# Kernel optimization log

Measured on AMD Instinct MI355X. Metric: run time of the kernel, lower is better.

## Reference

```python
import jax, jax.numpy as jnp
import numpy as np
import math

L = 6          # num_layers
D = 512        # hidden_dim
S = 2048       # seq_len
B = 8          # batch
ODIM = 1       # output_dim
SCALES = (24.0, 720.0)


def setup_inputs() -> dict:
    key = jax.random.key(0)
    ks = jax.random.split(key, 12)
    def n(k, shape, scale=0.02):
        return jax.random.normal(k, shape, dtype=jnp.float32) * scale
    return {
        "z": jax.random.normal(ks[0], (B, S, 1), dtype=jnp.float32),
        "c": jax.random.normal(ks[1], (B, S, 1), dtype=jnp.float32),
        "enc_w": n(ks[2], (D, 2)), "enc_b": jnp.zeros((D,), jnp.float32),
        "beta": jnp.ones((L, len(SCALES)), jnp.float32),
        "wq": n(ks[3], (L, D, D)), "bq": jnp.zeros((L, D), jnp.float32),
        "wk": n(ks[4], (L, D, D)), "bk": jnp.zeros((L, D), jnp.float32),
        "wv": n(ks[5], (L, D, D)), "bv": jnp.zeros((L, D), jnp.float32),
        "ln1_w": jnp.ones((L, D), jnp.float32), "ln1_b": jnp.zeros((L, D), jnp.float32),
        "ln2_w": jnp.ones((L, D), jnp.float32), "ln2_b": jnp.zeros((L, D), jnp.float32),
        "ff1_w": n(ks[6], (L, 4 * D, D)), "ff1_b": jnp.zeros((L, 4 * D), jnp.float32),
        "ff2_w": n(ks[7], (L, D, 4 * D)), "ff2_b": jnp.zeros((L, D), jnp.float32),
        "out_w": n(ks[8], (ODIM, D)), "out_b": jnp.zeros((ODIM,), jnp.float32),
    }


def _ln(x, w, b, eps=1e-5):
    m = jnp.mean(x, axis=-1, keepdims=True)
    v = jnp.var(x, axis=-1, keepdims=True)
    return (x - m) * jax.lax.rsqrt(v + eps) * w + b


def _posenc(seq_len, dim):
    pos = jnp.arange(seq_len, dtype=jnp.float32)[:, None]
    div = jnp.exp(jnp.arange(0, dim, 2, dtype=jnp.float32) * (-(math.log(10000.0) / dim)))
    pe = jnp.zeros((seq_len, dim), jnp.float32)
    pe = pe.at[:, 0::2].set(jnp.sin(pos * div))
    pe = pe.at[:, 1::2].set(jnp.cos(pos * div))
    return pe


def reference(z, c, enc_w, enc_b, beta, wq, bq, wk, bk, wv, bv,
              ln1_w, ln1_b, ln2_w, ln2_b, ff1_w, ff1_b, ff2_w, ff2_b,
              out_w, out_b):
    # SequenceEncoder: cat(z,c) -> Linear(2, D) -> + sinusoidal PE
    x = jnp.concatenate([z, c], axis=-1) @ enc_w.T + enc_b       # [B,S,D]
    seq_len, d = x.shape[1], x.shape[2]
    x = x + _posenc(seq_len, d)[None]
    sqrt_d = math.sqrt(d)

    idx = jnp.arange(seq_len, dtype=jnp.float32)
    dist = jnp.abs(idx[:, None] - idx[None, :])                  # [S,S]

    for l in range(L):
        # pre-norm with ln1 (applied twice in the original code - replicated)
        xn = _ln(x, ln1_w[l], ln1_b[l])
        Q = xn @ wq[l].T + bq[l]
        K = xn @ wk[l].T + bk[l]
        V = xn @ wv[l].T + bv[l]
        attn = jnp.einsum('bid,bjd->bij', Q, K) / sqrt_d          # [B,S,S]
        bias = beta[l, 0] * jnp.cos(2.0 * math.pi * dist / SCALES[0]) \
             + beta[l, 1] * jnp.cos(2.0 * math.pi * dist / SCALES[1])
        probs = jax.nn.softmax(attn + bias, axis=-1)
        att_out = jnp.einsum('bij,bjd->bid', probs, V)
        # original applies layer_norm_1 again to the residual sum
        x = _ln(x + att_out, ln1_w[l], ln1_b[l])
        xn2 = _ln(x, ln2_w[l], ln2_b[l])
        h = jax.nn.relu(xn2 @ ff1_w[l].T + ff1_b[l])
        x = x + h @ ff2_w[l].T + ff2_b[l]

    return x @ out_w.T + out_b                                    # [B,S,ODIM]
```

## Files before the change

### kernel.cpp

```cpp
#include <hip/hip_runtime.h>
#include <hip/hip_fp8.h>
#include <math.h>

#define BB 8
#define SS 2048
#define DD 512
#define LL 6
#define FFD 2048

typedef _Float16 half_t;
typedef __attribute__((ext_vector_type(8))) _Float16 half8;
typedef __attribute__((ext_vector_type(4))) float f32x4;

enum { EPI_NONE = 0, EPI_RELU = 2, EPI_RES = 3, EPI_ATTN = 4, EPI_QKV = 5, EPI_PV = 6 };

__device__ __forceinline__ unsigned char f2e4m3(float v) {
    __hip_fp8_e4m3 f(v);
    return f.__x;
}

__device__ __forceinline__ void gl_lds16(const void* g, void* l) {
    __builtin_amdgcn_global_load_lds(
        (const __attribute__((address_space(1))) unsigned int*)g,
        (__attribute__((address_space(3))) unsigned int*)l,
        16, 0, 0);
}

__device__ __forceinline__ void blockReduce2(float& a, float& b, float* sm) {
#pragma unroll
    for (int off = 32; off; off >>= 1) {
        a += __shfl_down(a, off);
        b += __shfl_down(b, off);
    }
    int lane = threadIdx.x & 63;
    int w = threadIdx.x >> 6;
    if (lane == 0) { sm[w] = a; sm[4 + w] = b; }
    __syncthreads();
    a = sm[0] + sm[1] + sm[2] + sm[3];
    b = sm[4] + sm[5] + sm[6] + sm[7];
    __syncthreads();
}

__global__ __launch_bounds__(256) void encode_kernel(
    const float* __restrict__ z, const float* __restrict__ c,
    const float* __restrict__ enc_w, const float* __restrict__ enc_b,
    float* __restrict__ x)
{
    int idx = blockIdx.x * 256 + threadIdx.x;
    int d  = idx & (DD - 1);
    int bs = idx >> 9;
    int s  = bs & (SS - 1);
    float v = z[bs] * enc_w[2 * d] + c[bs] * enc_w[2 * d + 1] + enc_b[d];
    float div = expf(-(float)(d & ~1) * (9.210340371976184f / 512.0f));
    float ang = (float)s * div;
    v += (d & 1) ? cosf(ang) : sinf(ang);
    x[idx] = v;
}

__global__ __launch_bounds__(256) void convert_ff_all_kernel(
    const float* __restrict__ f1, const float* __restrict__ f2,
    half_t* __restrict__ f1h, half_t* __restrict__ f2h)
{
    const size_t NF = (size_t)LL * FFD * DD;
    size_t i = (size_t)blockIdx.x * 256 + threadIdx.x;
    if (i < NF) f1h[i] = (half_t)f1[i];
    else        f2h[i - NF] = (half_t)f2[i - NF];
}

__global__ __launch_bounds__(256) void convert_qkv_kernel(
    const float* __restrict__ wq, const float* __restrict__ wk,
    const float* __restrict__ wv, half_t* __restrict__ wqkv)
{
    const int NQ = DD * DD;
    int i = blockIdx.x * 256 + threadIdx.x;
    int which = i >> 18, j = i & (NQ - 1);
    const float* s = (which == 0) ? wq : (which == 1) ? wk : wv;
    wqkv[i] = (half_t)s[j];
}

__global__ __launch_bounds__(256) void bias_table_kernel(
    const float* __restrict__ beta, float* __restrict__ tbl)
{
    int i = blockIdx.x * 256 + threadIdx.x;
    int l = i >> 11, d = i & (SS - 1);
    tbl[i] = beta[2 * l] * cosf(0.2617993877991494f * d)
           + beta[2 * l + 1] * cosf(0.008726646259971648f * d);
}

__global__ __launch_bounds__(256) void ln_kernel(
    const float* __restrict__ src, const float* __restrict__ w,
    const float* __restrict__ b, half_t* __restrict__ dst)
{
    __shared__ float sm[8];
    size_t row = blockIdx.x;
    const float* p = src + row * DD;
    int t = threadIdx.x;
    float v0 = p[t], v1 = p[t + 256];
    float s = v0 + v1, sq = v0 * v0 + v1 * v1;
    blockReduce2(s, sq, sm);
    float mean = s * (1.0f / DD);
    float var  = sq * (1.0f / DD) - mean * mean;
    float rs   = rsqrtf(var + 1e-5f);
    dst[row * DD + t]       = (half_t)((v0 - mean) * rs * w[t] + b[t]);
    dst[row * DD + t + 256] = (half_t)((v1 - mean) * rs * w[t + 256] + b[t + 256]);
}

__global__ __launch_bounds__(256) void ln_ln_kernel(
    float* __restrict__ x,
    const float* __restrict__ w1, const float* __restrict__ b1,
    const float* __restrict__ w2, const float* __restrict__ b2,
    half_t* __restrict__ xn)
{
    __shared__ float sm[8];
    size_t row = blockIdx.x;
    int t = threadIdx.x;
    float v0 = x[row * DD + t];
    float v1 = x[row * DD + t + 256];
    float s = v0 + v1, sq = v0 * v0 + v1 * v1;
    blockReduce2(s, sq, sm);
    float mean = s * (1.0f / DD);
    float var  = sq * (1.0f / DD) - mean * mean;
    float rs   = rsqrtf(var + 1e-5f);
    float y0 = (v0 - mean) * rs * w1[t] + b1[t];
    float y1 = (v1 - mean) * rs * w1[t + 256] + b1[t + 256];
    x[row * DD + t]       = y0;
    x[row * DD + t + 256] = y1;
    s = y0 + y1; sq = y0 * y0 + y1 * y1;
    blockReduce2(s, sq, sm);
    mean = s * (1.0f / DD);
    var  = sq * (1.0f / DD) - mean * mean;
    rs   = rsqrtf(var + 1e-5f);
    xn[row * DD + t]       = (half_t)((y0 - mean) * rs * w2[t] + b2[t]);
    xn[row * DD + t + 256] = (half_t)((y1 - mean) * rs * w2[t + 256] + b2[t + 256]);
}

template<typename TIN, int MT, int EPI, int SWZ = 0>
__global__ __launch_bounds__(256) void gemm_mfma(
    const void* __restrict__ Ap, const void* __restrict__ Wp,
    const float* __restrict__ bias, void* __restrict__ Cp,
    int N, int K, int Kst, float alpha,
    long long sA, long long sW, long long sC,
    const float* __restrict__ biasK, const float* __restrict__ biasV,
    unsigned char* __restrict__ Ck, unsigned char* __restrict__ Cv)
{
    constexpr int TM = MT / 32;
    constexpr int ES = (int)sizeof(TIN);
    constexpr int NS = 64 / (32 * ES);
    constexpr int ABYTES = MT * 64;
    constexpr int BBYTES = 128 * 64;
    __shared__ __align__(16) unsigned char As[2 * ABYTES];
    __shared__ __align__(16) unsigned char Bs[2 * BBYTES];

    int bxi, byi, bzi;
    if (SWZ == 1) {
        const int id = blockIdx.x;
        const int cc = id & 7, rr = id >> 3;
        bxi = rr & 15;
        const int ss = cc + 8 * (rr >> 4);
        byi = ss & 15; bzi = ss >> 4;
    } else { bxi = blockIdx.x; byi = blockIdx.y; bzi = blockIdx.z; }

    const int z = bzi;
    const unsigned char* A = (const unsigned char*)Ap + (size_t)z * sA * ES;
    const unsigned char* W = (const unsigned char*)Wp + (size_t)z * sW * ES;
    float*  Cf = (float*)Cp  + (size_t)z * sC;
    half_t* Ch = (half_t*)Cp + (size_t)z * sC;
    unsigned char* C8 = (unsigned char*)Cp + (size_t)z * sC;

    const int tid = threadIdx.x;
    const int wv = tid >> 6, ln = tid & 63;
    const int bm = bxi * MT, bn = byi * 128;
    const int wm = (wv & 1) * (MT / 2), wn = (wv >> 1) * 64;

    const int srow  = wv * 16 + (ln >> 2);
    const int scolB = (((ln & 3) ^ ((ln >> 3) & 3))) * 16;
    const unsigned char* Ag = A + (size_t)(bm + srow) * Kst * ES + scolB;
    const unsigned char* Bg = W + (size_t)(bn + srow) * Kst * ES + scolB;

    f32x4 acc[TM][4] = {};
    f32x4 accd[TM] = {};
    const long ONES8 = 0x3838383838383838L;

    const int lane15 = ln & 15, quad = ln >> 4;
    const int swr = (lane15 >> 1) & 3;
    const int nIter = (K * ES) / 64;

    {
        unsigned char* la = As + wv * 1024;
        unsigned char* lb = Bs + wv * 1024;
        gl_lds16(Ag, la);
        if (MT == 128) gl_lds16(Ag + (size_t)64 * Kst * ES, la + 4096);
        gl_lds16(Bg, lb);
        gl_lds16(Bg + (size_t)64 * Kst * ES, lb + 4096);
    }
    __syncthreads();

    for (int it = 0; it < nIter; ++it) {
        const int cur = it & 1;
        if (it + 1 < nIter) {
            const size_t ko = (size_t)(it + 1) * 64;
            unsigned char* la = As + (cur ^ 1) * ABYTES + wv * 1024;
            unsigned char* lb = Bs + (cur ^ 1) * BBYTES + wv * 1024;
            gl_lds16(Ag + ko, la);
            if (MT == 128) gl_lds16(Ag + (size_t)64 * Kst * ES + ko, la + 4096);
            gl_lds16(Bg + ko, lb);
            gl_lds16(Bg + (size_t)64 * Kst * ES + ko, lb + 4096);
        }

        const unsigned char* Ab = As + cur * ABYTES;
        const unsigned char* Bb = Bs + cur * BBYTES;

        if constexpr (ES == 2) {
            const int cB = (quad ^ swr) * 16;
            half8 aF[TM], bF[4];
#pragma unroll
            for (int i = 0; i < TM; ++i)
                aF[i] = *(const half8*)(Ab + (wm + i * 16 + lane15) * 64 + cB);
#pragma unroll
            for (int j = 0; j < 4; ++j)
                bF[j] = *(const half8*)(Bb + (wn + j * 16 + lane15) * 64 + cB);
#pragma unroll
            for (int i = 0; i < TM; ++i)
#pragma unroll
                for (int j = 0; j < 4; ++j)
                    acc[i][j] = __builtin_amdgcn_mfma_f32_16x16x32_f16(
                        aF[i], bF[j], acc[i][j], 0, 0, 0);
        } else {
            long aF8[NS][TM], bF8[NS][4];
#pragma unroll
            for (int s = 0; s < NS; ++s) {
                const int cB = (((s * 2 + (quad >> 1)) ^ swr) * 16) + (quad & 1) * 8;
#pragma unroll
                for (int i = 0; i < TM; ++i)
                    aF8[s][i] = *(const long*)(Ab + (wm + i * 16 + lane15) * 64 + cB);
#pragma unroll
                for (int j = 0; j < 4; ++j)
                    bF8[s][j] = *(const long*)(Bb + (wn + j * 16 + lane15) * 64 + cB);
            }
#pragma unroll
            for (int s = 0; s < NS; ++s)
#pragma unroll
                for (int i = 0; i < TM; ++i) {
#pragma unroll
                    for (int j = 0; j < 4; ++j)
                        acc[i][j] = __builtin_amdgcn_mfma_f32_16x16x32_fp8_fp8(
                            aF8[s][i], bF8[s][j], acc[i][j], 0, 0, 0);
                    if (EPI == EPI_PV)
                        accd[i] = __builtin_amdgcn_mfma_f32_16x16x32_fp8_fp8(
                            aF8[s][i], ONES8, accd[i], 0, 0, 0);
                }
        }

        __syncthreads();
    }

    float invd[TM][4];
    if (EPI == EPI_PV) {
#pragma unroll
        for (int i = 0; i < TM; ++i)
#pragma unroll
            for (int r = 0; r < 4; ++r)
                invd[i][r] = 1.0f / accd[i][r];
    }

#pragma unroll
    for (int i = 0; i < TM; ++i) {
        const int m0 = bm + wm + i * 16 + quad * 4;
#pragma unroll
        for (int j = 0; j < 4; ++j) {
            const int gn = bn + wn + j * 16 + lane15;
            if (EPI == EPI_QKV) {
                const int seg = gn >> 9, nn = gn & (DD - 1);
                if (seg == 2) {
                    unsigned int pk = 0;
#pragma unroll
                    for (int r = 0; r < 4; ++r)
                        pk |= (unsigned int)f2e4m3(acc[i][j][r] + biasV[nn]) << (8 * r);
                    const int b = m0 >> 11, s0 = m0 & (SS - 1);
                    *(unsigned int*)&Cv[((size_t)b * DD + nn) * SS + s0] = pk;
                } else {
                    const float bs = (seg == 0) ? bias[nn] : biasK[nn];
                    unsigned char* dst = (seg == 0) ? C8 : Ck;
#pragma unroll
                    for (int r = 0; r < 4; ++r)
                        dst[(size_t)(m0 + r) * DD + nn] = f2e4m3(acc[i][j][r] + bs);
                }
            } else {
#pragma unroll
                for (int r = 0; r < 4; ++r) {
                    const int gm = m0 + r;
                    float v = acc[i][j][r];
                    if (EPI == EPI_ATTN) {
                        int dist = gm - gn; if (dist < 0) dist = -dist;
                        v = __expf(fminf(v * alpha + bias[dist], 6.0f));
                        C8[(size_t)gm * N + gn] = f2e4m3(v);
                    } else if (EPI == EPI_PV) {
                        const size_t idx = (size_t)gm * N + gn;
                        Cf[idx] = v * invd[i][r] + Cf[idx];
                    } else if (EPI == EPI_RELU) {
                        Ch[(size_t)gm * N + gn] = (half_t)fmaxf(v + bias[gn], 0.0f);
                    } else {
                        const size_t idx = (size_t)gm * N + gn;
                        atomicAdd(&Cf[idx], v + (z == 0 ? bias[gn] : 0.0f));
                    }
                }
            }
        }
    }
}

__global__ __launch_bounds__(256) void out_kernel(
    const float* __restrict__ x, const float* __restrict__ ow,
    const float* __restrict__ ob, float* __restrict__ out)
{
    int row = blockIdx.x * 4 + (threadIdx.x >> 6);
    int lane = threadIdx.x & 63;
    const float* p = x + (size_t)row * DD;
    float s = 0.f;
#pragma unroll
    for (int k = 0; k < 8; ++k) s += p[lane + 64 * k] * ow[lane + 64 * k];
#pragma unroll
    for (int off = 32; off; off >>= 1) s += __shfl_down(s, off);
    if (lane == 0) out[row] = s + ob[0];
}

extern "C" void kernel_launch(void* const* d_in, const int* in_sizes, int n_in,
                              void* d_out, int out_size, void* d_ws, size_t ws_size,
                              hipStream_t stream)
{
    (void)in_sizes; (void)n_in; (void)out_size; (void)ws_size;
    const float* z     = (const float*)d_in[0];
    const float* c     = (const float*)d_in[1];
    const float* enc_w = (const float*)d_in[2];
    const float* enc_b = (const float*)d_in[3];
    const float* beta  = (const float*)d_in[4];
    const float* wq    = (const float*)d_in[5];
    const float* bq    = (const float*)d_in[6];
    const float* wk    = (const float*)d_in[7];
    const float* bk    = (const float*)d_in[8];
    const float* wv    = (const float*)d_in[9];
    const float* bv    = (const float*)d_in[10];
    const float* ln1w  = (const float*)d_in[11];
    const float* ln1b  = (const float*)d_in[12];
    const float* ln2w  = (const float*)d_in[13];
    const float* ln2b  = (const float*)d_in[14];
    const float* ff1w  = (const float*)d_in[15];
    const float* ff1b  = (const float*)d_in[16];
    const float* ff2w  = (const float*)d_in[17];
    const float* ff2b  = (const float*)d_in[18];
    const float* ow    = (const float*)d_in[19];
    const float* ob    = (const float*)d_in[20];

    const size_t BSD = (size_t)BB * SS * DD;
    const size_t BSS = (size_t)BB * SS * SS;
    const size_t NF  = (size_t)LL * FFD * DD;

    char* p = (char*)d_ws;
    float*  x    = (float*)p;  p += BSD * 4;
    half_t* xnh  = (half_t*)p; p += BSD * 2;
    unsigned char* sch = (unsigned char*)p; p += BSS;
    unsigned char* qh  = (unsigned char*)p; p += BSD;
    unsigned char* kh  = (unsigned char*)p; p += BSD;
    unsigned char* vth = (unsigned char*)p; p += BSD;
    half_t* hh   = (half_t*)p; p += (size_t)BB * SS * FFD * 2;
    half_t* wqkv = (half_t*)p; p += (size_t)3 * DD * DD * 2;
    half_t* f1h  = (half_t*)p; p += NF * 2;
    half_t* f2h  = (half_t*)p; p += NF * 2;
    float*  tbl  = (float*)p;

    const float alpha = 0.044194173824159216f;
    const int BS = BB * SS;
    const long long sQ = (long long)SS * DD, sP = (long long)SS * SS,
                    sV = (long long)DD * SS;

    bias_table_kernel<<<LL * SS / 256, 256, 0, stream>>>(beta, tbl);
    convert_ff_all_kernel<<<(int)(2 * NF / 256), 256, 0, stream>>>(ff1w, ff2w, f1h, f2h);
    encode_kernel<<<BS * DD / 256, 256, 0, stream>>>(z, c, enc_w, enc_b, x);

    for (int l = 0; l < LL; ++l) {
        convert_qkv_kernel<<<3 * DD * DD / 256, 256, 0, stream>>>(
            wq + (size_t)l * DD * DD, wk + (size_t)l * DD * DD,
            wv + (size_t)l * DD * DD, wqkv);

        ln_kernel<<<BS, 256, 0, stream>>>(x, ln1w + l * DD, ln1b + l * DD, xnh);

        gemm_mfma<half_t, 128, EPI_QKV><<<dim3(BS / 128, 12, 1), 256, 0, stream>>>(
            xnh, wqkv, bq + l * DD, qh, 1536, DD, DD, 0, 0, 0, 0,
            bk + l * DD, bv + l * DD, kh, vth);

        gemm_mfma<unsigned char, 128, EPI_ATTN, 1><<<dim3(2048, 1, 1), 256, 0, stream>>>(
            qh, kh, tbl + l * SS, sch, SS, DD, DD, alpha, sQ, sQ, sP,
            nullptr, nullptr, nullptr, nullptr);

        gemm_mfma<unsigned char, 64, EPI_PV><<<dim3(SS / 64, DD / 128, BB), 256, 0, stream>>>(
            sch, vth, nullptr, x, DD, SS, SS, 0, sP, sV, sQ,
            nullptr, nullptr, nullptr, nullptr);

        ln_ln_kernel<<<BS, 256, 0, stream>>>(x, ln1w + l * DD, ln1b + l * DD,
                                             ln2w + l * DD, ln2b + l * DD, xnh);

        gemm_mfma<half_t, 128, EPI_RELU><<<dim3(BS / 128, FFD / 128, 1), 256, 0, stream>>>(
            xnh, f1h + (size_t)l * FFD * DD, ff1b + l * FFD, hh, FFD, DD, DD, 0, 0, 0, 0,
            nullptr, nullptr, nullptr, nullptr);
        gemm_mfma<half_t, 64, EPI_RES><<<dim3(BS / 64, DD / 128, 2), 256, 0, stream>>>(
            hh, f2h + (size_t)l * DD * FFD, ff2b + l * DD, x, DD, FFD / 2, FFD, 0,
            FFD / 2, FFD / 2, 0,
            nullptr, nullptr, nullptr, nullptr);
    }

    out_kernel<<<BS / 4, 256, 0, stream>>>(x, ow, ob, (float*)d_out);
}
```

Baseline: 2.006 ms.

## Hoist QKV weight conversion, drop split-K FF2 atomics, alias activation buffers

All layers' QKV weights are now converted to fp16 once, inside a single merged conversion kernel, instead of one conversion launch per layer. The FF2 GEMM no longer splits K in two with atomicAdd; each block runs the full K=2048 and does a plain read-add-write residual store. The score, Q, K and V buffers now share memory with the FF hidden buffer, shrinking the workspace footprint. The trade-off is half as many FF2 blocks, which means less parallelism and a longer per-block K loop, in exchange for no atomic traffic and fewer launches.

```diff
diff --git a/kernel.cpp b/kernel.cpp
--- a/kernel.cpp
+++ b/kernel.cpp
@@ -57,25 +57,30 @@
     x[idx] = v;
 }
 
-__global__ __launch_bounds__(256) void convert_ff_all_kernel(
-    const float* __restrict__ f1, const float* __restrict__ f2,
+__global__ __launch_bounds__(256) void convert_all_kernel(
+    const float* __restrict__ wq, const float* __restrict__ wk,
+    const float* __restrict__ wv, const float* __restrict__ f1,
+    const float* __restrict__ f2, half_t* __restrict__ wqkv,
     half_t* __restrict__ f1h, half_t* __restrict__ f2h)
 {
-    const size_t NF = (size_t)LL * FFD * DD;
+    const size_t NQ  = (size_t)DD * DD;
+    const size_t NQ3 = 3 * (size_t)LL * NQ;
+    const size_t NF  = (size_t)LL * FFD * DD;
     size_t i = (size_t)blockIdx.x * 256 + threadIdx.x;
-    if (i < NF) f1h[i] = (half_t)f1[i];
-    else        f2h[i - NF] = (half_t)f2[i - NF];
-}
-
-__global__ __launch_bounds__(256) void convert_qkv_kernel(
-    const float* __restrict__ wq, const float* __restrict__ wk,
-    const float* __restrict__ wv, half_t* __restrict__ wqkv)
-{
-    const int NQ = DD * DD;
-    int i = blockIdx.x * 256 + threadIdx.x;
-    int which = i >> 18, j = i & (NQ - 1);
-    const float* s = (which == 0) ? wq : (which == 1) ? wk : wv;
-    wqkv[i] = (half_t)s[j];
+    if (i < NQ3) {
+        size_t l = i / (3 * NQ);
+        size_t r = i - l * 3 * NQ;
+        int which = (int)(r >> 18);
+        size_t j = r & (NQ - 1);
+        const float* s = (which == 0) ? wq : (which == 1) ? wk : wv;
+        wqkv[i] = (half_t)s[l * NQ + j];
+    } else if (i < NQ3 + NF) {
+        size_t k = i - NQ3;
+        f1h[k] = (half_t)f1[k];
+    } else if (i < NQ3 + 2 * NF) {
+        size_t k = i - NQ3 - NF;
+        f2h[k] = (half_t)f2[k];
+    }
 }
 
 __global__ __launch_bounds__(256) void bias_table_kernel(
@@ -138,7 +143,7 @@
 __global__ __launch_bounds__(256) void gemm_mfma(
     const void* __restrict__ Ap, const void* __restrict__ Wp,
     const float* __restrict__ bias, void* __restrict__ Cp,
-    int N, int K, int Kst, float alpha,
+    int N, int K, float alpha,
     long long sA, long long sW, long long sC,
     const float* __restrict__ biasK, const float* __restrict__ biasV,
     unsigned char* __restrict__ Ck, unsigned char* __restrict__ Cv)
@@ -174,8 +179,8 @@
 
     const int srow  = wv * 16 + (ln >> 2);
     const int scolB = (((ln & 3) ^ ((ln >> 3) & 3))) * 16;
-    const unsigned char* Ag = A + (size_t)(bm + srow) * Kst * ES + scolB;
-    const unsigned char* Bg = W + (size_t)(bn + srow) * Kst * ES + scolB;
+    const unsigned char* Ag = A + (size_t)(bm + srow) * K * ES + scolB;
+    const unsigned char* Bg = W + (size_t)(bn + srow) * K * ES + scolB;
 
     f32x4 acc[TM][4] = {};
     f32x4 accd[TM] = {};
@@ -189,9 +194,9 @@
         unsigned char* la = As + wv * 1024;
         unsigned char* lb = Bs + wv * 1024;
         gl_lds16(Ag, la);
-        if (MT == 128) gl_lds16(Ag + (size_t)64 * Kst * ES, la + 4096);
+        if (MT == 128) gl_lds16(Ag + (size_t)64 * K * ES, la + 4096);
         gl_lds16(Bg, lb);
-        gl_lds16(Bg + (size_t)64 * Kst * ES, lb + 4096);
+        gl_lds16(Bg + (size_t)64 * K * ES, lb + 4096);
     }
     __syncthreads();
 
@@ -202,9 +207,9 @@
             unsigned char* la = As + (cur ^ 1) * ABYTES + wv * 1024;
             unsigned char* lb = Bs + (cur ^ 1) * BBYTES + wv * 1024;
             gl_lds16(Ag + ko, la);
-            if (MT == 128) gl_lds16(Ag + (size_t)64 * Kst * ES + ko, la + 4096);
+            if (MT == 128) gl_lds16(Ag + (size_t)64 * K * ES + ko, la + 4096);
             gl_lds16(Bg + ko, lb);
-            gl_lds16(Bg + (size_t)64 * Kst * ES + ko, lb + 4096);
+            gl_lds16(Bg + (size_t)64 * K * ES + ko, lb + 4096);
         }
 
         const unsigned char* Ab = As + cur * ABYTES;
@@ -301,7 +306,7 @@
                         Ch[(size_t)gm * N + gn] = (half_t)fmaxf(v + bias[gn], 0.0f);
                     } else {
                         const size_t idx = (size_t)gm * N + gn;
-                        atomicAdd(&Cf[idx], v + (z == 0 ? bias[gn] : 0.0f));
+                        Cf[idx] = v + bias[gn] + Cf[idx];
                     }
                 }
             }
@@ -353,17 +358,19 @@
 
     const size_t BSD = (size_t)BB * SS * DD;
     const size_t BSS = (size_t)BB * SS * SS;
+    const size_t NQ  = (size_t)DD * DD;
     const size_t NF  = (size_t)LL * FFD * DD;
 
     char* p = (char*)d_ws;
     float*  x    = (float*)p;  p += BSD * 4;
     half_t* xnh  = (half_t*)p; p += BSD * 2;
-    unsigned char* sch = (unsigned char*)p; p += BSS;
-    unsigned char* qh  = (unsigned char*)p; p += BSD;
-    unsigned char* kh  = (unsigned char*)p; p += BSD;
-    unsigned char* vth = (unsigned char*)p; p += BSD;
-    half_t* hh   = (half_t*)p; p += (size_t)BB * SS * FFD * 2;
-    half_t* wqkv = (half_t*)p; p += (size_t)3 * DD * DD * 2;
+    char*   pool = p;          p += BSD * 2 * 4;
+    unsigned char* sch = (unsigned char*)pool;
+    unsigned char* qh  = (unsigned char*)(pool + BSS);
+    unsigned char* kh  = (unsigned char*)(pool + BSS + BSD);
+    unsigned char* vth = (unsigned char*)(pool + BSS + 2 * BSD);
+    half_t* hh   = (half_t*)pool;
+    half_t* wqkv = (half_t*)p; p += (size_t)3 * LL * NQ * 2;
     half_t* f1h  = (half_t*)p; p += NF * 2;
     half_t* f2h  = (half_t*)p; p += NF * 2;
     float*  tbl  = (float*)p;
@@ -373,38 +380,35 @@
     const long long sQ = (long long)SS * DD, sP = (long long)SS * SS,
                     sV = (long long)DD * SS;
 
+    const size_t convTotal = 3 * LL * NQ + 2 * NF;
     bias_table_kernel<<<LL * SS / 256, 256, 0, stream>>>(beta, tbl);
-    convert_ff_all_kernel<<<(int)(2 * NF / 256), 256, 0, stream>>>(ff1w, ff2w, f1h, f2h);
+    convert_all_kernel<<<(int)((convTotal + 255) / 256), 256, 0, stream>>>(
+        wq, wk, wv, ff1w, ff2w, wqkv, f1h, f2h);
     encode_kernel<<<BS * DD / 256, 256, 0, stream>>>(z, c, enc_w, enc_b, x);
 
     for (int l = 0; l < LL; ++l) {
-        convert_qkv_kernel<<<3 * DD * DD / 256, 256, 0, stream>>>(
-            wq + (size_t)l * DD * DD, wk + (size_t)l * DD * DD,
-            wv + (size_t)l * DD * DD, wqkv);
-
         ln_kernel<<<BS, 256, 0, stream>>>(x, ln1w + l * DD, ln1b + l * DD, xnh);
 
         gemm_mfma<half_t, 128, EPI_QKV><<<dim3(BS / 128, 12, 1), 256, 0, stream>>>(
-            xnh, wqkv, bq + l * DD, qh, 1536, DD, DD, 0, 0, 0, 0,
+            xnh, wqkv + (size_t)l * 3 * NQ, bq + l * DD, qh, 1536, DD, 0, 0, 0, 0,
             bk + l * DD, bv + l * DD, kh, vth);
 
         gemm_mfma<unsigned char, 128, EPI_ATTN, 1><<<dim3(2048, 1, 1), 256, 0, stream>>>(
-            qh, kh, tbl + l * SS, sch, SS, DD, DD, alpha, sQ, sQ, sP,
+            qh, kh, tbl + l * SS, sch, SS, DD, alpha, sQ, sQ, sP,
             nullptr, nullptr, nullptr, nullptr);
 
         gemm_mfma<unsigned char, 64, EPI_PV><<<dim3(SS / 64, DD / 128, BB), 256, 0, stream>>>(
-            sch, vth, nullptr, x, DD, SS, SS, 0, sP, sV, sQ,
+            sch, vth, nullptr, x, DD, SS, 0, sP, sV, sQ,
             nullptr, nullptr, nullptr, nullptr);
 
         ln_ln_kernel<<<BS, 256, 0, stream>>>(x, ln1w + l * DD, ln1b + l * DD,
                                              ln2w + l * DD, ln2b + l * DD, xnh);
 
         gemm_mfma<half_t, 128, EPI_RELU><<<dim3(BS / 128, FFD / 128, 1), 256, 0, stream>>>(
-            xnh, f1h + (size_t)l * FFD * DD, ff1b + l * FFD, hh, FFD, DD, DD, 0, 0, 0, 0,
+            xnh, f1h + (size_t)l * FFD * DD, ff1b + l * FFD, hh, FFD, DD, 0, 0, 0, 0,
             nullptr, nullptr, nullptr, nullptr);
-        gemm_mfma<half_t, 64, EPI_RES><<<dim3(BS / 64, DD / 128, 2), 256, 0, stream>>>(
-            hh, f2h + (size_t)l * DD * FFD, ff2b + l * DD, x, DD, FFD / 2, FFD, 0,
-            FFD / 2, FFD / 2, 0,
+        gemm_mfma<half_t, 64, EPI_RES><<<dim3(BS / 64, DD / 128, 1), 256, 0, stream>>>(
+            hh, f2h + (size_t)l * DD * FFD, ff2b + l * DD, x, DD, FFD, 0, 0, 0, 0,
             nullptr, nullptr, nullptr, nullptr);
     }
 
```

After: 1.898 ms. 1.06x faster.
